# Kernel optimization log

Measured on AMD Instinct MI355X. Metric: run time of the kernel, lower is better.

The kernel has to match this reference:

```python
import jax, jax.numpy as jnp
import numpy as np

B, I, H = 4096, 2048, 2048


def setup_inputs() -> dict:
    key = jax.random.key(0)
    k1, k2, k3, k4, k5 = jax.random.split(key, 5)
    return {
        "x": jax.random.normal(k1, (B, I), dtype=jnp.float32),
        "coefficients": jax.random.normal(k2, (I, H), dtype=jnp.float32) * 0.1,
        "amplitude_an": jax.random.normal(k3, (1, I, H), dtype=jnp.float32) * 0.1,
        "amplitude_bn": jax.random.normal(k4, (1, I, H), dtype=jnp.float32) * 0.1,
        "bias": jax.random.normal(k5, (1, I), dtype=jnp.float32),
    }


def reference(x, coefficients, amplitude_an, amplitude_bn, bias):
    # phase[b,h] = x[b,:] @ coefficients[:,h]  (same matmul done per-sample in torch loop)
    phase = x @ coefficients  # [B, H]
    num_harmonics = coefficients.shape[1]
    # sum over harmonics of an[i,h]*cos(phase[b,h]) + bn[i,h]*sin(phase[b,h])
    gain = (
        jnp.einsum("bh,ih->bi", jnp.cos(phase), amplitude_an[0])
        + jnp.einsum("bh,ih->bi", jnp.sin(phase), amplitude_bn[0])
        + num_harmonics * bias  # bias added per-harmonic before the sum over H
    )
    return gain  # [B, I]
```

## Files before the change

kernel.cpp:

```cpp
#include <hip/hip_runtime.h>
#include <hip/hip_bf16.h>

#define B_DIM 4096
#define I_DIM 2048
#define H_DIM 2048

typedef unsigned char u8;
typedef unsigned short u16;
typedef unsigned int u32;
typedef __attribute__((ext_vector_type(4))) float f32x4;
typedef __attribute__((ext_vector_type(4))) int i32x4;
typedef __attribute__((ext_vector_type(8))) int i32x8;

#define SBAR __builtin_amdgcn_sched_barrier(0)

__device__ __forceinline__ void gload_lds16(const void* g, void* l) {
  __builtin_amdgcn_global_load_lds(
      (const __attribute__((address_space(1))) void*)g,
      (__attribute__((address_space(3))) void*)l, 16, 0, 0);
}

__device__ __forceinline__ u32 f2fp4(float v, float inv_scale) {
  const float a = fabsf(v) * inv_scale;
  u32 m = (u32)(a > 0.25f) + (u32)(a > 0.75f) + (u32)(a > 1.25f) +
          (u32)(a > 1.75f) + (u32)(a > 2.5f) + (u32)(a > 3.5f) + (u32)(a > 5.0f);
  return ((__float_as_uint(v) >> 31) << 3) | m;
}

__global__ void prep_all(const float* __restrict__ x, const float* __restrict__ coeff,
                         const float* __restrict__ an, const float* __restrict__ bn,
                         u16* __restrict__ xf4, u16* __restrict__ ct4,
                         u32* __restrict__ ab4) {
  if (blockIdx.x < 512) {
    __shared__ float tile[32][33];
    const int tid = threadIdx.x;
    const int tx = tid & 31;
    const int ty = tid >> 5;
    const int hl = tid >> 3;
    const int q = (tid & 7) * 4;
#pragma unroll
    for (int rep = 0; rep < 8; ++rep) {
      const int tidx = blockIdx.x * 8 + rep;
      const int h0 = (tidx & 63) * 32;
      const int i0 = (tidx >> 6) * 32;
      for (int r = ty; r < 32; r += 8)
        tile[r][tx] = coeff[(long)(i0 + r) * H_DIM + (h0 + tx)];
      __syncthreads();
      u32 w = f2fp4(tile[q + 0][hl], 8.f) | (f2fp4(tile[q + 1][hl], 8.f) << 4) |
              (f2fp4(tile[q + 2][hl], 8.f) << 8) | (f2fp4(tile[q + 3][hl], 8.f) << 12);
      ct4[(long)(h0 + hl) * (I_DIM / 4) + ((i0 + q) >> 2)] = (u16)w;
      __syncthreads();
    }
    return;
  }
  const long NX4 = (long)B_DIM * I_DIM / 4;
  const long NA4 = (long)I_DIM * H_DIM / 4;
  const long total = NX4 + NA4;
  const long stride = (long)1024 * blockDim.x;
  for (long t = (long)(blockIdx.x - 512) * blockDim.x + threadIdx.x; t < total;
       t += stride) {
    if (t < NX4) {
      float4 v = *(const float4*)(x + t * 4);
      u32 b0 = f2fp4(v.x, 1.f) | (f2fp4(v.y, 1.f) << 4);
      u32 b1 = f2fp4(v.z, 1.f) | (f2fp4(v.w, 1.f) << 4);
      xf4[t] = (u16)(b0 | (b1 << 8));
    } else {
      long p = (t - NX4) * 4;
      float4 va = *(const float4*)(an + p);
      float4 vb = *(const float4*)(bn + p);
      u32 b0 = f2fp4(va.x, 8.f) | (f2fp4(vb.x, 8.f) << 4);
      u32 b1 = f2fp4(va.y, 8.f) | (f2fp4(vb.y, 8.f) << 4);
      u32 b2 = f2fp4(va.z, 8.f) | (f2fp4(vb.z, 8.f) << 4);
      u32 b3 = f2fp4(va.w, 8.f) | (f2fp4(vb.w, 8.f) << 4);
      ab4[p >> 2] = b0 | (b1 << 8) | (b2 << 16) | (b3 << 24);
    }
  }
}

__device__ __forceinline__ void stage_tile(const char* Ab, const char* Bb, long kbyte,
                                           long lda, long ldb, char* AsB, char* BsB,
                                           int tid) {
#pragma unroll
  for (int i = 0; i < 4; ++i) {
    const int o = i * 4096 + tid * 16;
    const int row = o >> 7;
    const int ls = ((((o >> 4) & 7) ^ (row & 7)) << 4);
    gload_lds16(Ab + (long)row * lda + kbyte + ls, AsB + o);
  }
#pragma unroll
  for (int i = 0; i < 4; ++i) {
    const int o = i * 4096 + tid * 16;
    const int row = o >> 7;
    const int ls = ((((o >> 4) & 7) ^ (row & 7)) << 4);
    gload_lds16(Bb + (long)row * ldb + kbyte + ls, BsB + o);
  }
}

__device__ __forceinline__ i32x4 frag_ld16(const char* S, int row, int slot) {
  return *(const i32x4*)(S + row * 128 + ((slot ^ (row & 7)) << 4));
}

template <int SA, int SB>
__device__ __forceinline__ void gemm_kloop_fp4(const char* __restrict__ A,
                                               const char* __restrict__ Bt,
                                               int rowA0, int colB0, long Kbytes,
                                               char* smem, f32x4 acc[4][4]) {
  const int tid = threadIdx.x;
  const int lane = tid & 63;
  const int wid = tid >> 6;
  const int wr = wid >> 1, wc = wid & 1;
  const long lda = Kbytes, ldb = Kbytes;
  const char* Ab = A + (long)rowA0 * lda;
  const char* Bb = Bt + (long)colB0 * ldb;
  const int arow = wr * 64 + (lane & 15);
  const int brow = wc * 64 + (lane & 15);
  const int g = lane >> 4;
  const int nt = (int)(Kbytes >> 7);
  char* AsB = smem;
  char* BsB = smem + 16384;

  stage_tile(Ab, Bb, 0, lda, ldb, AsB, BsB, tid);
  stage_tile(Ab, Bb, 128, lda, ldb, AsB + 32768, BsB + 32768, tid);

  for (int t = 0; t < nt; ++t) {
    const int cur = (t & 1) << 15;
    if (t < nt - 1) asm volatile("s_waitcnt vmcnt(8)" ::: "memory");
    else            asm volatile("s_waitcnt vmcnt(0)" ::: "memory");
    SBAR;
    __builtin_amdgcn_s_barrier();
    SBAR;

    i32x8 af[8], bfr[8];
#pragma unroll
    for (int s = 0; s < 2; ++s)
#pragma unroll
      for (int m = 0; m < 4; ++m) {
        *(i32x4*)&af[s * 4 + m]  = frag_ld16(AsB + cur, arow + m * 16, s * 4 + g);
        *(i32x4*)&bfr[s * 4 + m] = frag_ld16(BsB + cur, brow + m * 16, s * 4 + g);
      }
    asm volatile("s_waitcnt lgkmcnt(0)" ::: "memory");
    SBAR;
    __builtin_amdgcn_s_barrier();
    SBAR;

    if (t + 2 < nt)
      stage_tile(Ab, Bb, (long)(t + 2) * 128, lda, ldb, AsB + cur, BsB + cur, tid);

    __builtin_amdgcn_s_setprio(1);
#pragma unroll
    for (int s = 0; s < 2; ++s)
#pragma unroll
      for (int m = 0; m < 4; ++m)
#pragma unroll
        for (int n = 0; n < 4; ++n)
          acc[m][n] = __builtin_amdgcn_mfma_scale_f32_16x16x128_f8f6f4(
              af[s * 4 + m], bfr[s * 4 + n], acc[m][n], 4, 4, 0, SA, 0, SB);
    __builtin_amdgcn_s_setprio(0);
    SBAR;
  }
}

__device__ __forceinline__ void tile_xy(int& bx, int& by) {
  const int bid = blockIdx.x;
  const int xcd = bid & 7;
  const int loc = bid >> 3;
  const int cy = xcd >> 1;
  const int cx = xcd & 1;
  by = cy * 8 + (loc >> 3);
  bx = cx * 8 + (loc & 7);
}

__global__ __launch_bounds__(256) void gemm_phase(const char* __restrict__ xf4,
                                                  const char* __restrict__ ct4,
                                                  u8* __restrict__ cs4) {
  __shared__ __align__(16) char smem[65536];
  int bx, by;
  tile_xy(bx, by);
  const int rowA0 = by * 128;
  const int colB0 = bx * 128;
  f32x4 acc[4][4];
#pragma unroll
  for (int m = 0; m < 4; ++m)
#pragma unroll
    for (int n = 0; n < 4; ++n)
#pragma unroll
      for (int j = 0; j < 4; ++j) acc[m][n][j] = 0.0f;

  gemm_kloop_fp4<0x7F7F7F7F, 0x7C7C7C7C>(xf4, ct4, rowA0, colB0, I_DIM / 2, smem, acc);

  const int lane = threadIdx.x & 63;
  const int wid = threadIdx.x >> 6;
  const int wr = wid >> 1, wc = wid & 1;
#pragma unroll
  for (int m = 0; m < 4; ++m) {
#pragma unroll
    for (int n = 0; n < 4; ++n) {
      const int col = colB0 + wc * 64 + n * 16 + (lane & 15);
#pragma unroll
      for (int j = 0; j < 4; ++j) {
        const int row = rowA0 + wr * 64 + m * 16 + (lane >> 4) * 4 + j;
        const float p = acc[m][n][j];
        float sp, cp;
        __sincosf(p, &sp, &cp);
        const u32 b = f2fp4(cp, 4.f) | (f2fp4(sp, 4.f) << 4);
        cs4[(long)row * H_DIM + col] = (u8)b;
      }
    }
  }
}

__global__ __launch_bounds__(256) void gemm_gain(const char* __restrict__ cs4,
                                                 const char* __restrict__ ab4,
                                                 const float* __restrict__ bias,
                                                 float* __restrict__ out) {
  __shared__ __align__(16) char smem[65536];
  int bx, by;
  tile_xy(bx, by);
  const int rowA0 = by * 128;
  const int colB0 = bx * 128;
  f32x4 acc[4][4];
#pragma unroll
  for (int m = 0; m < 4; ++m)
#pragma unroll
    for (int n = 0; n < 4; ++n)
#pragma unroll
      for (int j = 0; j < 4; ++j) acc[m][n][j] = 0.0f;

  gemm_kloop_fp4<0x7D7D7D7D, 0x7C7C7C7C>(cs4, ab4, rowA0, colB0, H_DIM, smem, acc);

  const int lane = threadIdx.x & 63;
  const int wid = threadIdx.x >> 6;
  const int wr = wid >> 1, wc = wid & 1;
#pragma unroll
  for (int m = 0; m < 4; ++m) {
#pragma unroll
    for (int n = 0; n < 4; ++n) {
      const int col = colB0 + wc * 64 + n * 16 + (lane & 15);
      const float bv = 2048.0f * bias[col];
#pragma unroll
      for (int j = 0; j < 4; ++j) {
        const int row = rowA0 + wr * 64 + m * 16 + (lane >> 4) * 4 + j;
        out[(long)row * I_DIM + col] = acc[m][n][j] + bv;
      }
    }
  }
}

extern "C" void kernel_launch(void* const* d_in, const int* in_sizes, int n_in,
                              void* d_out, int out_size, void* d_ws, size_t ws_size,
                              hipStream_t stream) {
  const float* x     = (const float*)d_in[0];
  const float* coeff = (const float*)d_in[1];
  const float* an    = (const float*)d_in[2];
  const float* bn    = (const float*)d_in[3];
  const float* bias  = (const float*)d_in[4];
  float* out = (float*)d_out;

  char* ws = (char*)d_ws;
  char* xf4 = ws;
  char* ct4 = ws + (4L << 20);
  char* ab4 = ws + (8L << 20);
  u8*  cs4  = (u8*)(ws + (12L << 20));

  prep_all<<<1536, 256, 0, stream>>>(x, coeff, an, bn, (u16*)xf4, (u16*)ct4,
                                     (u32*)ab4);
  gemm_phase<<<512, 256, 0, stream>>>(xf4, ct4, cs4);
  gemm_gain<<<512, 256, 0, stream>>>((const char*)cs4, (const char*)ab4, bias, out);
}
```

Baseline: 62.62 us.

## Fuse phase and gain GEMMs into one kernel with per-row-strip spin barriers

Merges the two GEMM kernels into one persistent launch. Each block computes its phase tile, then waits on an atomic counter until all 16 blocks of its 128-row strip have written their cos/sin tile before starting the gain GEMM on that strip. This removes a kernel launch boundary and the full-grid drain between the two stages. The cost is spin-waiting and the need for all 512 blocks to be co-resident, which the launch bound of two blocks per CU is meant to ensure; if they are not all resident the kernel can deadlock.

```diff
diff --git a/kernel.cpp b/kernel.cpp
--- a/kernel.cpp
+++ b/kernel.cpp
@@ -30,8 +30,9 @@
 __global__ void prep_all(const float* __restrict__ x, const float* __restrict__ coeff,
                          const float* __restrict__ an, const float* __restrict__ bn,
                          u16* __restrict__ xf4, u16* __restrict__ ct4,
-                         u32* __restrict__ ab4) {
+                         u32* __restrict__ ab4, u32* __restrict__ strip_done) {
   if (blockIdx.x < 512) {
+    if (blockIdx.x == 0 && threadIdx.x < 32) strip_done[threadIdx.x] = 0;
     __shared__ float tile[32][33];
     const int tid = threadIdx.x;
     const int tx = tid & 31;
@@ -170,77 +171,85 @@
   bx = cx * 8 + (loc & 7);
 }
 
-__global__ __launch_bounds__(256) void gemm_phase(const char* __restrict__ xf4,
-                                                  const char* __restrict__ ct4,
-                                                  u8* __restrict__ cs4) {
+__global__ __launch_bounds__(256, 2) void phase_gain(
+    const char* __restrict__ xf4, const char* __restrict__ ct4,
+    u8* __restrict__ cs4, const char* __restrict__ ab4,
+    const float* __restrict__ bias, float* __restrict__ out,
+    u32* __restrict__ strip_done) {
   __shared__ __align__(16) char smem[65536];
   int bx, by;
   tile_xy(bx, by);
   const int rowA0 = by * 128;
   const int colB0 = bx * 128;
-  f32x4 acc[4][4];
-#pragma unroll
-  for (int m = 0; m < 4; ++m)
-#pragma unroll
-    for (int n = 0; n < 4; ++n)
-#pragma unroll
-      for (int j = 0; j < 4; ++j) acc[m][n][j] = 0.0f;
-
-  gemm_kloop_fp4<0x7F7F7F7F, 0x7C7C7C7C>(xf4, ct4, rowA0, colB0, I_DIM / 2, smem, acc);
-
   const int lane = threadIdx.x & 63;
   const int wid = threadIdx.x >> 6;
   const int wr = wid >> 1, wc = wid & 1;
-#pragma unroll
-  for (int m = 0; m < 4; ++m) {
-#pragma unroll
-    for (int n = 0; n < 4; ++n) {
-      const int col = colB0 + wc * 64 + n * 16 + (lane & 15);
-#pragma unroll
-      for (int j = 0; j < 4; ++j) {
-        const int row = rowA0 + wr * 64 + m * 16 + (lane >> 4) * 4 + j;
-        const float p = acc[m][n][j];
-        float sp, cp;
-        __sincosf(p, &sp, &cp);
-        const u32 b = f2fp4(cp, 4.f) | (f2fp4(sp, 4.f) << 4);
-        cs4[(long)row * H_DIM + col] = (u8)b;
+
+  {
+    f32x4 acc[4][4];
+#pragma unroll
+    for (int m = 0; m < 4; ++m)
+#pragma unroll
+      for (int n = 0; n < 4; ++n)
+#pragma unroll
+        for (int j = 0; j < 4; ++j) acc[m][n][j] = 0.0f;
+
+    gemm_kloop_fp4<0x7F7F7F7F, 0x7C7C7C7C>(xf4, ct4, rowA0, colB0, I_DIM / 2, smem,
+                                           acc);
+
+#pragma unroll
+    for (int m = 0; m < 4; ++m) {
+#pragma unroll
+      for (int n = 0; n < 4; ++n) {
+        const int col = colB0 + wc * 64 + n * 16 + (lane & 15);
+#pragma unroll
+        for (int j = 0; j < 4; ++j) {
+          const int row = rowA0 + wr * 64 + m * 16 + (lane >> 4) * 4 + j;
+          const float p = acc[m][n][j];
+          float sp, cp;
+          __sincosf(p, &sp, &cp);
+          const u32 b = f2fp4(cp, 4.f) | (f2fp4(sp, 4.f) << 4);
+          cs4[(long)row * H_DIM + col] = (u8)b;
+        }
       }
     }
   }
-}
-
-__global__ __launch_bounds__(256) void gemm_gain(const char* __restrict__ cs4,
-                                                 const char* __restrict__ ab4,
-                                                 const float* __restrict__ bias,
-                                                 float* __restrict__ out) {
-  __shared__ __align__(16) char smem[65536];
-  int bx, by;
-  tile_xy(bx, by);
-  const int rowA0 = by * 128;
-  const int colB0 = bx * 128;
-  f32x4 acc[4][4];
-#pragma unroll
-  for (int m = 0; m < 4; ++m)
-#pragma unroll
-    for (int n = 0; n < 4; ++n)
-#pragma unroll
-      for (int j = 0; j < 4; ++j) acc[m][n][j] = 0.0f;
-
-  gemm_kloop_fp4<0x7D7D7D7D, 0x7C7C7C7C>(cs4, ab4, rowA0, colB0, H_DIM, smem, acc);
-
-  const int lane = threadIdx.x & 63;
-  const int wid = threadIdx.x >> 6;
-  const int wr = wid >> 1, wc = wid & 1;
-#pragma unroll
-  for (int m = 0; m < 4; ++m) {
-#pragma unroll
-    for (int n = 0; n < 4; ++n) {
-      const int col = colB0 + wc * 64 + n * 16 + (lane & 15);
-      const float bv = 2048.0f * bias[col];
-#pragma unroll
-      for (int j = 0; j < 4; ++j) {
-        const int row = rowA0 + wr * 64 + m * 16 + (lane >> 4) * 4 + j;
-        out[(long)row * I_DIM + col] = acc[m][n][j] + bv;
+
+  __threadfence();
+  __syncthreads();
+  if (threadIdx.x == 0) {
+    __hip_atomic_fetch_add(&strip_done[by], 1u, __ATOMIC_ACQ_REL,
+                           __HIP_MEMORY_SCOPE_AGENT);
+    while (__hip_atomic_load(&strip_done[by], __ATOMIC_ACQUIRE,
+                             __HIP_MEMORY_SCOPE_AGENT) < 16u)
+      __builtin_amdgcn_s_sleep(1);
+  }
+  __syncthreads();
+  __threadfence();
+
+  {
+    f32x4 acc[4][4];
+#pragma unroll
+    for (int m = 0; m < 4; ++m)
+#pragma unroll
+      for (int n = 0; n < 4; ++n)
+#pragma unroll
+        for (int j = 0; j < 4; ++j) acc[m][n][j] = 0.0f;
+
+    gemm_kloop_fp4<0x7D7D7D7D, 0x7C7C7C7C>((const char*)cs4, ab4, rowA0, colB0,
+                                           H_DIM, smem, acc);
+
+#pragma unroll
+    for (int m = 0; m < 4; ++m) {
+#pragma unroll
+      for (int n = 0; n < 4; ++n) {
+        const int col = colB0 + wc * 64 + n * 16 + (lane & 15);
+        const float bv = 2048.0f * bias[col];
+#pragma unroll
+        for (int j = 0; j < 4; ++j) {
+          const int row = rowA0 + wr * 64 + m * 16 + (lane >> 4) * 4 + j;
+          out[(long)row * I_DIM + col] = acc[m][n][j] + bv;
+        }
       }
     }
   }
@@ -261,9 +270,10 @@
   char* ct4 = ws + (4L << 20);
   char* ab4 = ws + (8L << 20);
   u8*  cs4  = (u8*)(ws + (12L << 20));
+  u32* strip_done = (u32*)(ws + (20L << 20));
 
   prep_all<<<1536, 256, 0, stream>>>(x, coeff, an, bn, (u16*)xf4, (u16*)ct4,
-                                     (u32*)ab4);
-  gemm_phase<<<512, 256, 0, stream>>>(xf4, ct4, cs4);
-  gemm_gain<<<512, 256, 0, stream>>>((const char*)cs4, (const char*)ab4, bias, out);
-}
+                                     (u32*)ab4, strip_done);
+  phase_gain<<<512, 256, 0, stream>>>(xf4, ct4, cs4, (const char*)ab4, bias, out,
+                                      strip_done);
+}
```

Result: slower. 164.6 us (+162.8%).
